# Kernel tuning notes

Hardware: AMD Instinct MI355X
Metric: run time of the kernel (lower is better)

## Reference

```python
import jax, jax.numpy as jnp
import numpy as np

B, S, D_MODEL, H = 256, 128, 1024, 8
DK = D_MODEL // H      # 128; source code implicitly requires S == DK == P
P = 128                # number of relative positions (2k+1)
SCALE = 1.0 / np.sqrt(DK * 3.0)  # scale_factor = 3 (c2c + p2c + c2p all present)
NEG = -1.0e9


def setup_inputs() -> dict:
    rng = jax.random.key(0)
    ks = jax.random.split(rng, 16)
    n = lambda k, sh, s=1.0: jax.random.normal(k, sh, dtype=jnp.float32) * s
    return {
        "query": n(ks[0], (B, S, D_MODEL)),
        "key": n(ks[1], (B, S, D_MODEL)),
        "value": n(ks[2], (B, S, D_MODEL)),
        "q_pos_indices": jax.random.randint(ks[3], (B, H, S, S), 0, P, dtype=jnp.int32),
        "kv_pos_indices": jax.random.randint(ks[4], (B, H, S, S), 0, P, dtype=jnp.int32),
        "rel_q": n(ks[5], (1, H, P, DK), 0.02),
        "rel_k": n(ks[6], (1, H, P, DK), 0.02),
        "rel_v": n(ks[7], (1, H, P, DK), 0.02),
        "Wq": n(ks[8], (D_MODEL, D_MODEL), 0.02), "bq": jnp.zeros((D_MODEL,), jnp.float32),
        "Wk": n(ks[9], (D_MODEL, D_MODEL), 0.02), "bk": jnp.zeros((D_MODEL,), jnp.float32),
        "Wv": n(ks[10], (D_MODEL, D_MODEL), 0.02), "bv": jnp.zeros((D_MODEL,), jnp.float32),
        "Wo": n(ks[11], (D_MODEL, D_MODEL), 0.02), "bo": jnp.zeros((D_MODEL,), jnp.float32),
    }


def _forward(query, key, value, q_pos, kv_pos, rel_q, rel_k, rel_v,
             Wq, bq, Wk, bk, Wv, bv, Wo, bo):
    def split(x):  # [B,S,D] -> [B,H,S,DK]
        return x.reshape(B, S, H, DK).transpose(0, 2, 1, 3)

    q = split(query @ Wq + bq)
    k = split(key @ Wk + bk)
    v = split(value @ Wv + bv)

    # content-to-content
    c2c = jnp.einsum('bhid,bhjd->bhij', q, k) * SCALE
    # position-to-content: rel_q @ k^T -> [B,H,P,S], gather over P with q_pos
    p2c = jnp.einsum('hpd,bhjd->bhpj', rel_q[0], k) * SCALE
    p2c = jnp.take_along_axis(p2c, q_pos, axis=2)          # [B,H,S,S]
    # content-to-position: q @ rel_k^T -> [B,H,S,P], gather over P with kv_pos
    c2p = jnp.einsum('bhid,hpd->bhip', q, rel_k[0]) * SCALE
    c2p = jnp.take_along_axis(c2p, kv_pos, axis=3)         # [B,H,S,S]

    scores = c2c + p2c + c2p
    # source subtracts (detached) rowwise max BEFORE masking
    scores = scores - jax.lax.stop_gradient(scores.max(axis=-1, keepdims=True))

    # mask = (pos_indices == 0), with first seq_len flattened entries (row 0) forced True;
    # masked_fill(mask == 0, -1e9) keeps entries where mask is True
    mask = (q_pos == 0)
    mask = mask.at[:, :, 0, :].set(True)
    scores = jnp.where(mask, scores, NEG)

    probs = jax.nn.softmax(scores, axis=-1)  # dropout inactive (eval / p=0)

    ctx = jnp.einsum('bhij,bhjd->bhid', probs, v)          # [B,H,S,DK]
    # value-side positional path (valid because P == S == DK in this module)
    pos_ctx = jnp.einsum('bhij,hjd->bhid', probs, rel_v[0])
    pos_ctx = jnp.take_along_axis(pos_ctx, kv_pos, axis=3)
    ctx = ctx + pos_ctx

    out = ctx.transpose(0, 2, 1, 3).reshape(B, S, D_MODEL)
    return out @ Wo + bo


def reference(query, key, value, q_pos_indices, kv_pos_indices, rel_q, rel_k, rel_v,
              Wq, bq, Wk, bk, Wv, bv, Wo, bo):
    return _forward(query, key, value, q_pos_indices, kv_pos_indices,
                    rel_q, rel_k, rel_v, Wq, bq, Wk, bk, Wv, bv, Wo, bo)
```

## Files before the change

### kernel.cpp

```cpp
#include <hip/hip_runtime.h>
#include <cstdint>
#include <cstddef>

typedef __bf16 bf16;
typedef __attribute__((ext_vector_type(8))) __bf16 bf16x8;
typedef __attribute__((ext_vector_type(4))) float f32x4;

#define NB 256
#define NS 128
#define NH 8
#define NDK 128
#define NP 128
#define NDM 1024

static constexpr float kScale = 0.05103103630798287f;
static constexpr float kNeg = -1.0e9f;

static __device__ __forceinline__ f32x4 mfma16(bf16x8 a, bf16x8 b, f32x4 c) {
  return __builtin_amdgcn_mfma_f32_16x16x32_bf16(a, b, c, 0, 0, 0);
}

static __device__ __forceinline__ void gld_lds16(const bf16* g, bf16* l) {
  __builtin_amdgcn_global_load_lds(
      (const __attribute__((address_space(1))) void*)g,
      (__attribute__((address_space(3))) void*)l, 16, 0, 0);
}

static __device__ __forceinline__ float red16_max(float v) {
  v = fmaxf(v, __shfl_xor(v, 1, 64));
  v = fmaxf(v, __shfl_xor(v, 2, 64));
  v = fmaxf(v, __shfl_xor(v, 4, 64));
  v = fmaxf(v, __shfl_xor(v, 8, 64));
  return v;
}
static __device__ __forceinline__ float red16_sum(float v) {
  v += __shfl_xor(v, 1, 64);
  v += __shfl_xor(v, 2, 64);
  v += __shfl_xor(v, 4, 64);
  v += __shfl_xor(v, 8, 64);
  return v;
}

static __device__ void transpose64(const float* __restrict__ src, bf16* __restrict__ dst,
                                   int rows, int cols, int r0, int c0,
                                   float (*t)[65], int tid) {
  const int tr = tid >> 4, tc = tid & 15;
#pragma unroll
  for (int i = 0; i < 4; i++) {
    int r = tr + i * 16;
    float4 v = *(const float4*)&src[(size_t)(r0 + r) * cols + c0 + tc * 4];
    t[r][tc * 4 + 0] = v.x;
    t[r][tc * 4 + 1] = v.y;
    t[r][tc * 4 + 2] = v.z;
    t[r][tc * 4 + 3] = v.w;
  }
  __syncthreads();
#pragma unroll
  for (int i = 0; i < 4; i++) {
    int c = tr + i * 16;
    union { bf16 o[4]; uint64_t u; } pk;
#pragma unroll
    for (int k2 = 0; k2 < 4; k2++) pk.o[k2] = (bf16)t[tc * 4 + k2][c];
    *(uint64_t*)&dst[(size_t)(c0 + c) * rows + r0 + tc * 4] = pk.u;
  }
}

__global__ __launch_bounds__(256) void prep_kernel(
    const float* __restrict__ Wq, const float* __restrict__ Wk,
    const float* __restrict__ Wv, const float* __restrict__ Wo,
    const float* __restrict__ rel_q, const float* __restrict__ rel_k,
    const float* __restrict__ rel_v,
    bf16* __restrict__ Wtq, bf16* __restrict__ Wtk,
    bf16* __restrict__ Wtv, bf16* __restrict__ Wto,
    bf16* __restrict__ rqb, bf16* __restrict__ rkb, bf16* __restrict__ rvt) {
  __shared__ float t[64][65];
  const int tid = threadIdx.x;
  const int z = blockIdx.z;
  if (z < 4) {
    const float* src = (z == 0) ? Wq : (z == 1) ? Wk : (z == 2) ? Wv : Wo;
    bf16* dst = (z == 0) ? Wtq : (z == 1) ? Wtk : (z == 2) ? Wtv : Wto;
    transpose64(src, dst, NDM, NDM, blockIdx.y * 64, blockIdx.x * 64, t, tid);
  } else if (z == 4) {
    int lb = blockIdx.y * 16 + blockIdx.x;
    if (lb < 32) {
      int hh = lb >> 2, tt = lb & 3;
      transpose64(rel_v + (size_t)hh * NP * NDK, rvt + (size_t)hh * NDK * NP,
                  NP, NDK, (tt >> 1) * 64, (tt & 1) * 64, t, tid);
    }
  } else {
    int lb = blockIdx.y * 16 + blockIdx.x;
    if (lb < 128) {
      size_t base = (size_t)lb * 1024 + (size_t)tid * 4;
      float4 a = *(const float4*)&rel_q[base];
      float4 c = *(const float4*)&rel_k[base];
      union { bf16 o[4]; uint64_t u; } pa, pc;
      pa.o[0] = (bf16)a.x; pa.o[1] = (bf16)a.y; pa.o[2] = (bf16)a.z; pa.o[3] = (bf16)a.w;
      pc.o[0] = (bf16)c.x; pc.o[1] = (bf16)c.y; pc.o[2] = (bf16)c.z; pc.o[3] = (bf16)c.w;
      *(uint64_t*)&rqb[base] = pa.u;
      *(uint64_t*)&rkb[base] = pc.u;
    }
  }
}

__global__ __launch_bounds__(256) void cast_kernel(
    const float* __restrict__ x0, const float* __restrict__ x1,
    const float* __restrict__ x2,
    bf16* __restrict__ y0, bf16* __restrict__ y1, bf16* __restrict__ y2) {
  const int z = blockIdx.z;
  const float* x = (z == 0) ? x0 : (z == 1) ? x1 : x2;
  bf16* y = (z == 0) ? y0 : (z == 1) ? y1 : y2;
  size_t i = ((size_t)blockIdx.x * 256 + threadIdx.x) * 8;
  float4 a = *(const float4*)&x[i];
  float4 b = *(const float4*)&x[i + 4];
  union { bf16 o[8]; bf16x8 v; } u;
  u.o[0] = (bf16)a.x; u.o[1] = (bf16)a.y; u.o[2] = (bf16)a.z; u.o[3] = (bf16)a.w;
  u.o[4] = (bf16)b.x; u.o[5] = (bf16)b.y; u.o[6] = (bf16)b.z; u.o[7] = (bf16)b.w;
  *(bf16x8*)&y[i] = u.v;
}

__global__ __launch_bounds__(256) void proj_gemm(
    const bf16* __restrict__ Xq, const bf16* __restrict__ Xk, const bf16* __restrict__ Xv,
    const bf16* __restrict__ Wtq, const bf16* __restrict__ Wtk, const bf16* __restrict__ Wtv,
    const float* __restrict__ bq, const float* __restrict__ bk, const float* __restrict__ bv,
    bf16* __restrict__ Oq, bf16* __restrict__ Ok, bf16* __restrict__ Ov) {
  __shared__ __attribute__((aligned(16))) bf16 sA[128 * 64];
  __shared__ __attribute__((aligned(16))) bf16 sB[128 * 64];
  const int z = blockIdx.z;
  const bf16* X = (z == 0) ? Xq : (z == 1) ? Xk : Xv;
  const bf16* Wt = (z == 0) ? Wtq : (z == 1) ? Wtk : Wtv;
  const float* bias = (z == 0) ? bq : (z == 1) ? bk : bv;
  bf16* O = (z == 0) ? Oq : (z == 1) ? Ok : Ov;

  const int M0 = blockIdx.y * 128, N0 = blockIdx.x * 128;
  const int tid = threadIdx.x, lane = tid & 63, w = tid >> 6;
  const int l15 = lane & 15, l4 = lane >> 4;
  const int wm = w >> 1, wn = w & 1;

  f32x4 acc[4][4];
#pragma unroll
  for (int mt = 0; mt < 4; mt++)
#pragma unroll
    for (int nt = 0; nt < 4; nt++) acc[mt][nt] = (f32x4){0.f, 0.f, 0.f, 0.f};

  const int lr = lane >> 3, lc = (lane & 7) * 8;
  const bf16* ap[4];
  const bf16* bp[4];
#pragma unroll
  for (int i = 0; i < 4; i++) {
    int row = w * 32 + i * 8 + lr;
    ap[i] = X + (size_t)(M0 + row) * NDM + lc;
    bp[i] = Wt + (size_t)(N0 + row) * NDM + lc;
  }

  for (int k0 = 0; k0 < NDM; k0 += 64) {
#pragma unroll
    for (int i = 0; i < 4; i++) {
      int chunk = w * 4 + i;
      gld_lds16(ap[i], sA + chunk * 512);
      gld_lds16(bp[i], sB + chunk * 512);
      ap[i] += 64;
      bp[i] += 64;
    }
    __syncthreads();
#pragma unroll
    for (int kk = 0; kk < 64; kk += 32) {
      bf16x8 af[4], bfv[4];
#pragma unroll
      for (int mt = 0; mt < 4; mt++)
        af[mt] = *(const bf16x8*)&sA[(wm * 64 + mt * 16 + l15) * 64 + kk + l4 * 8];
#pragma unroll
      for (int nt = 0; nt < 4; nt++)
        bfv[nt] = *(const bf16x8*)&sB[(wn * 64 + nt * 16 + l15) * 64 + kk + l4 * 8];
#pragma unroll
      for (int mt = 0; mt < 4; mt++)
#pragma unroll
        for (int nt = 0; nt < 4; nt++)
          acc[mt][nt] = mfma16(af[mt], bfv[nt], acc[mt][nt]);
    }
    __syncthreads();
  }
#pragma unroll
  for (int mt = 0; mt < 4; mt++) {
#pragma unroll
    for (int nt = 0; nt < 4; nt++) {
      int n = N0 + wn * 64 + nt * 16 + l15;
      float bv_ = bias[n];
      int h = n >> 7, dk = n & 127;
#pragma unroll
      for (int r = 0; r < 4; r++) {
        int m = M0 + wm * 64 + mt * 16 + l4 * 4 + r;
        int b = m >> 7, s = m & 127;
        O[(((size_t)b * NH + h) * NS + s) * NDK + dk] = (bf16)(acc[mt][nt][r] + bv_);
      }
    }
  }
}

__global__ __launch_bounds__(256) void out_gemm(
    const bf16* __restrict__ Ax, const bf16* __restrict__ Wt,
    const float* __restrict__ bias, float* __restrict__ Out) {
  __shared__ __attribute__((aligned(16))) bf16 sA[128 * 64];
  __shared__ __attribute__((aligned(16))) bf16 sB[128 * 64];
  const int M0 = blockIdx.y * 128, N0 = blockIdx.x * 128;
  const int tid = threadIdx.x, lane = tid & 63, w = tid >> 6;
  const int l15 = lane & 15, l4 = lane >> 4;
  const int wm = w >> 1, wn = w & 1;

  f32x4 acc[4][4];
#pragma unroll
  for (int mt = 0; mt < 4; mt++)
#pragma unroll
    for (int nt = 0; nt < 4; nt++) acc[mt][nt] = (f32x4){0.f, 0.f, 0.f, 0.f};

  const int lr = lane >> 3, lc = (lane & 7) * 8;
  const bf16* ap[4];
  const bf16* bp[4];
#pragma unroll
  for (int i = 0; i < 4; i++) {
    int row = w * 32 + i * 8 + lr;
    ap[i] = Ax + (size_t)(M0 + row) * NDM + lc;
    bp[i] = Wt + (size_t)(N0 + row) * NDM + lc;
  }

  for (int k0 = 0; k0 < NDM; k0 += 64) {
#pragma unroll
    for (int i = 0; i < 4; i++) {
      int chunk = w * 4 + i;
      gld_lds16(ap[i], sA + chunk * 512);
      gld_lds16(bp[i], sB + chunk * 512);
      ap[i] += 64;
      bp[i] += 64;
    }
    __syncthreads();
#pragma unroll
    for (int kk = 0; kk < 64; kk += 32) {
      bf16x8 af[4], bfv[4];
#pragma unroll
      for (int mt = 0; mt < 4; mt++)
        af[mt] = *(const bf16x8*)&sA[(wm * 64 + mt * 16 + l15) * 64 + kk + l4 * 8];
#pragma unroll
      for (int nt = 0; nt < 4; nt++)
        bfv[nt] = *(const bf16x8*)&sB[(wn * 64 + nt * 16 + l15) * 64 + kk + l4 * 8];
#pragma unroll
      for (int mt = 0; mt < 4; mt++)
#pragma unroll
        for (int nt = 0; nt < 4; nt++)
          acc[mt][nt] = mfma16(af[mt], bfv[nt], acc[mt][nt]);
    }
    __syncthreads();
  }
#pragma unroll
  for (int mt = 0; mt < 4; mt++) {
#pragma unroll
    for (int nt = 0; nt < 4; nt++) {
      int n = N0 + wn * 64 + nt * 16 + l15;
      float bv_ = bias[n];
#pragma unroll
      for (int r = 0; r < 4; r++) {
        int m = M0 + wm * 64 + mt * 16 + l4 * 4 + r;
        Out[(size_t)m * NDM + n] = acc[mt][nt][r] + bv_;
      }
    }
  }
}

__global__ __launch_bounds__(256) void vt_kernel(const bf16* __restrict__ Vin,
                                                 bf16* __restrict__ Vt) {
  __shared__ __attribute__((aligned(16))) bf16 t[64][72];
  const size_t base = (size_t)blockIdx.z * (NS * NDK);
  const int r0 = blockIdx.y * 64, c0 = blockIdx.x * 64;
  const int tid = threadIdx.x;
  const int tr = tid >> 3, tc8 = tid & 7;
#pragma unroll
  for (int i = 0; i < 2; i++) {
    int r = tr + i * 32;
    *(bf16x8*)&t[r][tc8 * 8] = *(const bf16x8*)&Vin[base + (size_t)(r0 + r) * NDK + c0 + tc8 * 8];
  }
  __syncthreads();
#pragma unroll
  for (int i = 0; i < 2; i++) {
    int c = tr + i * 32;
    bf16x8 o;
#pragma unroll
    for (int k2 = 0; k2 < 8; k2++) o[k2] = t[tc8 * 8 + k2][c];
    *(bf16x8*)&Vt[base + (size_t)(c0 + c) * NS + r0 + tc8 * 8] = o;
  }
}

__global__ __launch_bounds__(256, 1) void attn_kernel(
    const bf16* __restrict__ Qg, const bf16* __restrict__ Kg, const bf16* __restrict__ Vtg,
    const bf16* __restrict__ relq, const bf16* __restrict__ relk, const bf16* __restrict__ relvT,
    const int* __restrict__ qpos, const int* __restrict__ kvpos,
    bf16* __restrict__ ctx) {
  constexpr int LD = 136;
  __shared__ __attribute__((aligned(16))) bf16 R0[128 * LD];
  __shared__ __attribute__((aligned(16))) bf16 R1[128 * LD];
  __shared__ __attribute__((aligned(16))) bf16 R2[128 * LD];
  __shared__ __attribute__((aligned(16))) bf16 R3[128 * LD];

  const int bh = blockIdx.x;
  const int b = bh >> 3, h = bh & 7;
  const int tid = threadIdx.x, lane = tid & 63, w = tid >> 6;
  const int l15 = lane & 15, l4 = lane >> 4;
  const int m0 = w * 32;

  const size_t tb = (size_t)bh * (NS * NDK);
  const bf16* Qp = Qg + tb;
  const bf16* Kp = Kg + tb;
  const bf16* Vp = Vtg + tb;
  const bf16* rq = relq + (size_t)h * NP * NDK;
  const bf16* rk = relk + (size_t)h * NP * NDK;
  const bf16* rv = relvT + (size_t)h * NDK * NP;
  const int* qpp = qpos + (size_t)bh * NS * NS;
  const int* kpp = kvpos + (size_t)bh * NS * NS;

  auto load_tile = [&](bf16* dst, const bf16* src) {
    const int r = tid >> 4, c8 = tid & 15;
#pragma unroll
    for (int i = 0; i < 8; i++) {
      int rr = r + i * 16;
      *(bf16x8*)&dst[rr * LD + c8 * 8] = *(const bf16x8*)&src[rr * 128 + c8 * 8];
    }
  };
  auto gemmNT = [&](const bf16* A, const bf16* Bm, f32x4 (&acc)[2][8]) {
#pragma unroll
    for (int kk = 0; kk < 128; kk += 32) {
      bf16x8 a0 = *(const bf16x8*)&A[(m0 + l15) * LD + kk + l4 * 8];
      bf16x8 a1 = *(const bf16x8*)&A[(m0 + 16 + l15) * LD + kk + l4 * 8];
#pragma unroll
      for (int nt = 0; nt < 8; nt++) {
        bf16x8 bb = *(const bf16x8*)&Bm[(nt * 16 + l15) * LD + kk + l4 * 8];
        acc[0][nt] = mfma16(a0, bb, acc[0][nt]);
        acc[1][nt] = mfma16(a1, bb, acc[1][nt]);
      }
    }
  };

  load_tile(R0, Qp);
  load_tile(R1, Kp);
  load_tile(R2, rq);
  __syncthreads();

  {
    f32x4 acc[2][8];
#pragma unroll
    for (int mt = 0; mt < 2; mt++)
#pragma unroll
      for (int nt = 0; nt < 8; nt++) acc[mt][nt] = (f32x4){0.f, 0.f, 0.f, 0.f};
    gemmNT(R2, R1, acc);
#pragma unroll
    for (int mt = 0; mt < 2; mt++)
#pragma unroll
      for (int nt = 0; nt < 8; nt++)
#pragma unroll
        for (int r = 0; r < 4; r++) {
          int pp = m0 + mt * 16 + l4 * 4 + r;
          int j = nt * 16 + l15;
          R3[pp * LD + j] = (bf16)(acc[mt][nt][r] * kScale);
        }
  }
  f32x4 sc[2][8];
#pragma unroll
  for (int mt = 0; mt < 2; mt++)
#pragma unroll
    for (int nt = 0; nt < 8; nt++) sc[mt][nt] = (f32x4){0.f, 0.f, 0.f, 0.f};
  gemmNT(R0, R1, sc);
  __syncthreads();

  load_tile(R2, rk);
  __syncthreads();

  {
    f32x4 acc[2][8];
#pragma unroll
    for (int mt = 0; mt < 2; mt++)
#pragma unroll
      for (int nt = 0; nt < 8; nt++) acc[mt][nt] = (f32x4){0.f, 0.f, 0.f, 0.f};
    gemmNT(R0, R2, acc);
#pragma unroll
    for (int mt = 0; mt < 2; mt++)
#pragma unroll
      for (int nt = 0; nt < 8; nt++)
#pragma unroll
        for (int r = 0; r < 4; r++) {
          int i = m0 + mt * 16 + l4 * 4 + r;
          int pp = nt * 16 + l15;
          R1[i * LD + pp] = (bf16)(acc[mt][nt][r] * kScale);
        }
  }

  unsigned long long keep = 0ull;
#pragma unroll
  for (int mt = 0; mt < 2; mt++)
#pragma unroll
    for (int nt = 0; nt < 8; nt++)
#pragma unroll
      for (int r = 0; r < 4; r++) {
        int i = m0 + mt * 16 + l4 * 4 + r;
        int j = nt * 16 + l15;
        int qv = qpp[i * NS + j];
        int kv = kpp[i * NS + j];
        float v = sc[mt][nt][r] * kScale + (float)R3[qv * LD + j] + (float)R1[i * LD + kv];
        sc[mt][nt][r] = v;
        if (qv == 0 || i == 0) keep |= 1ull << (mt * 32 + nt * 4 + r);
      }
  float rmx[2][4];
#pragma unroll
  for (int mt = 0; mt < 2; mt++)
#pragma unroll
    for (int r = 0; r < 4; r++) {
      float m = -3.0e38f;
#pragma unroll
      for (int nt = 0; nt < 8; nt++) m = fmaxf(m, sc[mt][nt][r]);
      rmx[mt][r] = red16_max(m);
    }
#pragma unroll
  for (int mt = 0; mt < 2; mt++)
#pragma unroll
    for (int nt = 0; nt < 8; nt++)
#pragma unroll
      for (int r = 0; r < 4; r++) {
        float v = sc[mt][nt][r] - rmx[mt][r];
        if (!((keep >> (mt * 32 + nt * 4 + r)) & 1ull)) v = kNeg;
        sc[mt][nt][r] = v;
      }
  float m2[2][4], inv[2][4];
#pragma unroll
  for (int mt = 0; mt < 2; mt++)
#pragma unroll
    for (int r = 0; r < 4; r++) {
      float m = -3.0e38f;
#pragma unroll
      for (int nt = 0; nt < 8; nt++) m = fmaxf(m, sc[mt][nt][r]);
      m2[mt][r] = red16_max(m);
    }
#pragma unroll
  for (int mt = 0; mt < 2; mt++)
#pragma unroll
    for (int nt = 0; nt < 8; nt++)
#pragma unroll
      for (int r = 0; r < 4; r++) sc[mt][nt][r] = __expf(sc[mt][nt][r] - m2[mt][r]);
#pragma unroll
  for (int mt = 0; mt < 2; mt++)
#pragma unroll
    for (int r = 0; r < 4; r++) {
      float s = 0.f;
#pragma unroll
      for (int nt = 0; nt < 8; nt++) s += sc[mt][nt][r];
      inv[mt][r] = 1.0f / red16_sum(s);
    }
#pragma unroll
  for (int mt = 0; mt < 2; mt++)
#pragma unroll
    for (int nt = 0; nt < 8; nt++)
#pragma unroll
      for (int r = 0; r < 4; r++) sc[mt][nt][r] *= inv[mt][r];
  __syncthreads();

#pragma unroll
  for (int mt = 0; mt < 2; mt++)
#pragma unroll
    for (int nt = 0; nt < 8; nt++)
#pragma unroll
      for (int r = 0; r < 4; r++) {
        int i = m0 + mt * 16 + l4 * 4 + r;
        int j = nt * 16 + l15;
        R3[i * LD + j] = (bf16)sc[mt][nt][r];
      }
  load_tile(R0, Vp);
  load_tile(R1, rv);
  __syncthreads();

  {
    f32x4 acc2[2][8];
#pragma unroll
    for (int mt = 0; mt < 2; mt++)
#pragma unroll
      for (int nt = 0; nt < 8; nt++) acc2[mt][nt] = (f32x4){0.f, 0.f, 0.f, 0.f};
    gemmNT(R3, R1, acc2);
#pragma unroll
    for (int mt = 0; mt < 2; mt++)
#pragma unroll
      for (int nt = 0; nt < 8; nt++)
#pragma unroll
        for (int r = 0; r < 4; r++) {
          int i = m0 + mt * 16 + l4 * 4 + r;
          int d = nt * 16 + l15;
          R2[i * LD + d] = (bf16)acc2[mt][nt][r];
        }
  }
  {
    f32x4 acc1[2][8];
#pragma unroll
    for (int mt = 0; mt < 2; mt++)
#pragma unroll
      for (int nt = 0; nt < 8; nt++) acc1[mt][nt] = (f32x4){0.f, 0.f, 0.f, 0.f};
    gemmNT(R3, R0, acc1);
#pragma unroll
    for (int mt = 0; mt < 2; mt++)
#pragma unroll
      for (int nt = 0; nt < 8; nt++)
#pragma unroll
        for (int r = 0; r < 4; r++) {
          int i = m0 + mt * 16 + l4 * 4 + r;
          int d = nt * 16 + l15;
          int kv = kpp[i * NS + d];
          float v = acc1[mt][nt][r] + (float)R2[i * LD + kv];
          ctx[(((size_t)b * NS + i) * NH + h) * NDK + d] = (bf16)v;
        }
  }
}

extern "C" void kernel_launch(void* const* d_in, const int* in_sizes, int n_in,
                              void* d_out, int out_size, void* d_ws, size_t ws_size,
                              hipStream_t stream) {
  const float* query = (const float*)d_in[0];
  const float* key   = (const float*)d_in[1];
  const float* value = (const float*)d_in[2];
  const int* qpos    = (const int*)d_in[3];
  const int* kvpos   = (const int*)d_in[4];
  const float* rel_q = (const float*)d_in[5];
  const float* rel_k = (const float*)d_in[6];
  const float* rel_v = (const float*)d_in[7];
  const float* Wq = (const float*)d_in[8];
  const float* bq = (const float*)d_in[9];
  const float* Wk = (const float*)d_in[10];
  const float* bk = (const float*)d_in[11];
  const float* Wv = (const float*)d_in[12];
  const float* bv = (const float*)d_in[13];
  const float* Wo = (const float*)d_in[14];
  const float* bo = (const float*)d_in[15];
  float* out = (float*)d_out;

  char* p = (char*)d_ws;
  size_t off = 0;
  auto take = [&](size_t n) {
    char* r = p + off;
    off += (n + 255) & ~(size_t)255;
    return r;
  };
  bf16* Wtq = (bf16*)take((size_t)NDM * NDM * 2);
  bf16* Wtk = (bf16*)take((size_t)NDM * NDM * 2);
  bf16* Wtv = (bf16*)take((size_t)NDM * NDM * 2);
  bf16* Wto = (bf16*)take((size_t)NDM * NDM * 2);
  bf16* rqb = (bf16*)take((size_t)NH * NP * NDK * 2);
  bf16* rkb = (bf16*)take((size_t)NH * NP * NDK * 2);
  bf16* rvt = (bf16*)take((size_t)NH * NDK * NP * 2);
  const size_t big = (size_t)NB * NH * NS * NDK * 2;
  bf16* qws  = (bf16*)take(big);
  bf16* kws  = (bf16*)take(big);
  bf16* vws  = (bf16*)take(big);
  bf16* vtws = (bf16*)take(big);
  bf16* ctxw = (bf16*)take(big);
  bf16* xtra = (bf16*)take(big);
  bf16* xq = vtws;
  bf16* xk = ctxw;
  bf16* xv = xtra;

  hipLaunchKernelGGL(prep_kernel, dim3(16, 16, 6), dim3(256), 0, stream,
                     Wq, Wk, Wv, Wo, rel_q, rel_k, rel_v,
                     Wtq, Wtk, Wtv, Wto, rqb, rkb, rvt);
  hipLaunchKernelGGL(cast_kernel, dim3((NB * NS * NDM) / (256 * 8), 1, 3), dim3(256), 0, stream,
                     query, key, value, xq, xk, xv);
  hipLaunchKernelGGL(proj_gemm, dim3(8, 256, 3), dim3(256), 0, stream,
                     xq, xk, xv, Wtq, Wtk, Wtv, bq, bk, bv, qws, kws, vws);
  hipLaunchKernelGGL(vt_kernel, dim3(2, 2, NB * NH), dim3(256), 0, stream, vws, vtws);
  hipLaunchKernelGGL(attn_kernel, dim3(NB * NH), dim3(256), 0, stream,
                     qws, kws, vtws, rqb, rkb, rvt, qpos, kvpos, ctxw);
  hipLaunchKernelGGL(out_gemm, dim3(8, 256), dim3(256), 0, stream, ctxw, Wto, bo, out);
}
```

Measured before the change: 1.210 ms.

## Replace projection and output GEMMs with 256x256 double-buffered pipelined kernel

Merges the two GEMM kernels into one templated kernel that uses 256x256 tiles, 512 threads, and double-buffered LDS. Global loads for the next tile are interleaved between MFMA phases, with explicit waitcnt, barriers and setprio. It also XOR-swizzles the LDS layout to avoid bank conflicts and remaps block order so neighbouring blocks share L2 data. The aim is more operand reuse and overlap of memory with compute, at the cost of heavy register pressure and many barriers.

```diff
diff --git a/kernel.cpp b/kernel.cpp
--- a/kernel.cpp
+++ b/kernel.cpp
@@ -24,6 +24,12 @@
   __builtin_amdgcn_global_load_lds(
       (const __attribute__((address_space(1))) void*)g,
       (__attribute__((address_space(3))) void*)l, 16, 0, 0);
+}
+
+static __device__ __forceinline__ void barx() {
+  __builtin_amdgcn_sched_barrier(0);
+  __builtin_amdgcn_s_barrier();
+  __builtin_amdgcn_sched_barrier(0);
 }
 
 static __device__ __forceinline__ float red16_max(float v) {
@@ -118,147 +124,165 @@
   *(bf16x8*)&y[i] = u.v;
 }
 
-__global__ __launch_bounds__(256) void proj_gemm(
-    const bf16* __restrict__ Xq, const bf16* __restrict__ Xk, const bf16* __restrict__ Xv,
-    const bf16* __restrict__ Wtq, const bf16* __restrict__ Wtk, const bf16* __restrict__ Wtv,
-    const float* __restrict__ bq, const float* __restrict__ bk, const float* __restrict__ bv,
-    bf16* __restrict__ Oq, bf16* __restrict__ Ok, bf16* __restrict__ Ov) {
-  __shared__ __attribute__((aligned(16))) bf16 sA[128 * 64];
-  __shared__ __attribute__((aligned(16))) bf16 sB[128 * 64];
+#define TSZ (256 * 64)
+
+template <int MODE>
+__global__ __launch_bounds__(512, 2) void gemm256(
+    const bf16* __restrict__ X0, const bf16* __restrict__ X1, const bf16* __restrict__ X2,
+    const bf16* __restrict__ W0, const bf16* __restrict__ W1, const bf16* __restrict__ W2,
+    const float* __restrict__ b0p, const float* __restrict__ b1p, const float* __restrict__ b2p,
+    bf16* __restrict__ Obf0, bf16* __restrict__ Obf1, bf16* __restrict__ Obf2,
+    float* __restrict__ Of32) {
+  __shared__ __attribute__((aligned(16))) bf16 sA[2 * TSZ];
+  __shared__ __attribute__((aligned(16))) bf16 sB[2 * TSZ];
+
   const int z = blockIdx.z;
-  const bf16* X = (z == 0) ? Xq : (z == 1) ? Xk : Xv;
-  const bf16* Wt = (z == 0) ? Wtq : (z == 1) ? Wtk : Wtv;
-  const float* bias = (z == 0) ? bq : (z == 1) ? bk : bv;
-  bf16* O = (z == 0) ? Oq : (z == 1) ? Ok : Ov;
-
-  const int M0 = blockIdx.y * 128, N0 = blockIdx.x * 128;
+  const bf16* X  = (MODE == 1) ? X0 : ((z == 0) ? X0 : (z == 1) ? X1 : X2);
+  const bf16* Wt = (MODE == 1) ? W0 : ((z == 0) ? W0 : (z == 1) ? W1 : W2);
+  const float* bias = (MODE == 1) ? b0p : ((z == 0) ? b0p : (z == 1) ? b1p : b2p);
+
+  const int nx = gridDim.x;
+  const int flat = blockIdx.y * nx + blockIdx.x;
+  const int cpx = (nx * gridDim.y) >> 3;
+  const int swz = (flat & 7) * cpx + (flat >> 3);
+  const int M0 = (swz / nx) * 256;
+  const int N0 = (swz % nx) * 256;
+
   const int tid = threadIdx.x, lane = tid & 63, w = tid >> 6;
   const int l15 = lane & 15, l4 = lane >> 4;
-  const int wm = w >> 1, wn = w & 1;
-
-  f32x4 acc[4][4];
-#pragma unroll
-  for (int mt = 0; mt < 4; mt++)
+  const int wm = w >> 2, wn = w & 3;
+
+  const int lr = lane >> 3;
+  const int scol = ((lane & 7) ^ lr) * 8;
+  const size_t aRow = (size_t)(M0 + w * 16 + lr) * NDM + scol;
+  const size_t bRow = (size_t)(N0 + w * 16 + lr) * NDM + scol;
+  bf16* const dA = sA + (w * 16) * 64;
+  bf16* const dB = sB + (w * 16) * 64;
+
+  auto stA = [&](int bufi, int half, int t) {
+    const bf16* s = X + aRow + (size_t)half * 128 * NDM + t * 64;
+    bf16* d = dA + bufi * TSZ + half * (128 * 64);
+    gld_lds16(s, d);
+    gld_lds16(s + 8 * NDM, d + 8 * 64);
+  };
+  auto stB = [&](int bufi, int half, int t) {
+    const bf16* s = Wt + bRow + (size_t)half * 128 * NDM + t * 64;
+    bf16* d = dB + bufi * TSZ + half * (128 * 64);
+    gld_lds16(s, d);
+    gld_lds16(s + 8 * NDM, d + 8 * 64);
+  };
+
+  f32x4 acc[8][4];
+#pragma unroll
+  for (int mt = 0; mt < 8; mt++)
 #pragma unroll
     for (int nt = 0; nt < 4; nt++) acc[mt][nt] = (f32x4){0.f, 0.f, 0.f, 0.f};
 
-  const int lr = lane >> 3, lc = (lane & 7) * 8;
-  const bf16* ap[4];
-  const bf16* bp[4];
-#pragma unroll
-  for (int i = 0; i < 4; i++) {
-    int row = w * 32 + i * 8 + lr;
-    ap[i] = X + (size_t)(M0 + row) * NDM + lc;
-    bp[i] = Wt + (size_t)(N0 + row) * NDM + lc;
-  }
-
-  for (int k0 = 0; k0 < NDM; k0 += 64) {
-#pragma unroll
-    for (int i = 0; i < 4; i++) {
-      int chunk = w * 4 + i;
-      gld_lds16(ap[i], sA + chunk * 512);
-      gld_lds16(bp[i], sB + chunk * 512);
-      ap[i] += 64;
-      bp[i] += 64;
-    }
-    __syncthreads();
-#pragma unroll
-    for (int kk = 0; kk < 64; kk += 32) {
-      bf16x8 af[4], bfv[4];
-#pragma unroll
-      for (int mt = 0; mt < 4; mt++)
-        af[mt] = *(const bf16x8*)&sA[(wm * 64 + mt * 16 + l15) * 64 + kk + l4 * 8];
-#pragma unroll
-      for (int nt = 0; nt < 4; nt++)
-        bfv[nt] = *(const bf16x8*)&sB[(wn * 64 + nt * 16 + l15) * 64 + kk + l4 * 8];
-#pragma unroll
-      for (int mt = 0; mt < 4; mt++)
-#pragma unroll
-        for (int nt = 0; nt < 4; nt++)
-          acc[mt][nt] = mfma16(af[mt], bfv[nt], acc[mt][nt]);
-    }
-    __syncthreads();
-  }
-#pragma unroll
-  for (int mt = 0; mt < 4; mt++) {
-#pragma unroll
-    for (int nt = 0; nt < 4; nt++) {
-      int n = N0 + wn * 64 + nt * 16 + l15;
-      float bv_ = bias[n];
-      int h = n >> 7, dk = n & 127;
-#pragma unroll
-      for (int r = 0; r < 4; r++) {
-        int m = M0 + wm * 64 + mt * 16 + l4 * 4 + r;
-        int b = m >> 7, s = m & 127;
-        O[(((size_t)b * NH + h) * NS + s) * NDK + dk] = (bf16)(acc[mt][nt][r] + bv_);
+  const int kc0 = (l4 * 8) ^ ((l15 & 7) * 8);
+  const int kc1 = (32 + l4 * 8) ^ ((l15 & 7) * 8);
+  int arow[8], brow[4];
+#pragma unroll
+  for (int mt = 0; mt < 8; mt++) arow[mt] = (wm * 128 + mt * 16 + l15) * 64;
+#pragma unroll
+  for (int nt = 0; nt < 4; nt++) brow[nt] = (wn * 64 + nt * 16 + l15) * 64;
+
+  stA(0, 0, 0); stA(0, 1, 0); stB(0, 0, 0); stB(0, 1, 0);
+
+  const int NT = NDM / 64;
+  for (int t = 0; t < NT; ++t) {
+    const int cur = t & 1, nxt = cur ^ 1;
+    const bf16* cA = sA + cur * TSZ;
+    const bf16* cB = sB + cur * TSZ;
+    const bool pf = (t + 1 < NT);
+
+    if (pf) {
+      stA(nxt, 0, t + 1);
+      asm volatile("s_waitcnt vmcnt(2)" ::: "memory");
+    } else {
+      asm volatile("s_waitcnt vmcnt(0)" ::: "memory");
+    }
+    barx();
+    bf16x8 a0[8], b0[4], a1[8], b1[4];
+#pragma unroll
+    for (int mt = 0; mt < 4; mt++) a0[mt] = *(const bf16x8*)&cA[arow[mt] + kc0];
+#pragma unroll
+    for (int nt = 0; nt < 4; nt++) b0[nt] = *(const bf16x8*)&cB[brow[nt] + kc0];
+#pragma unroll
+    for (int mt = 4; mt < 8; mt++) a0[mt] = *(const bf16x8*)&cA[arow[mt] + kc0];
+    __builtin_amdgcn_s_setprio(1);
+#pragma unroll
+    for (int mt = 0; mt < 4; mt++)
+#pragma unroll
+      for (int nt = 0; nt < 4; nt++) acc[mt][nt] = mfma16(a0[mt], b0[nt], acc[mt][nt]);
+    __builtin_amdgcn_s_setprio(0);
+    barx();
+
+#pragma unroll
+    for (int mt = 0; mt < 4; mt++) a1[mt] = *(const bf16x8*)&cA[arow[mt] + kc1];
+    if (pf) stA(nxt, 1, t + 1);
+    barx();
+    __builtin_amdgcn_s_setprio(1);
+#pragma unroll
+    for (int mt = 4; mt < 8; mt++)
+#pragma unroll
+      for (int nt = 0; nt < 4; nt++) acc[mt][nt] = mfma16(a0[mt], b0[nt], acc[mt][nt]);
+    __builtin_amdgcn_s_setprio(0);
+    barx();
+
+#pragma unroll
+    for (int nt = 0; nt < 4; nt++) b1[nt] = *(const bf16x8*)&cB[brow[nt] + kc1];
+#pragma unroll
+    for (int mt = 4; mt < 8; mt++) a1[mt] = *(const bf16x8*)&cA[arow[mt] + kc1];
+    if (pf) stB(nxt, 0, t + 1);
+    barx();
+    __builtin_amdgcn_s_setprio(1);
+#pragma unroll
+    for (int mt = 0; mt < 4; mt++)
+#pragma unroll
+      for (int nt = 0; nt < 4; nt++) acc[mt][nt] = mfma16(a1[mt], b1[nt], acc[mt][nt]);
+    __builtin_amdgcn_s_setprio(0);
+    barx();
+
+    if (pf) stB(nxt, 1, t + 1);
+    barx();
+    __builtin_amdgcn_s_setprio(1);
+#pragma unroll
+    for (int mt = 4; mt < 8; mt++)
+#pragma unroll
+      for (int nt = 0; nt < 4; nt++) acc[mt][nt] = mfma16(a1[mt], b1[nt], acc[mt][nt]);
+    __builtin_amdgcn_s_setprio(0);
+    barx();
+  }
+
+  if (MODE == 0) {
+    bf16* O = (z == 0) ? Obf0 : (z == 1) ? Obf1 : Obf2;
+#pragma unroll
+    for (int mt = 0; mt < 8; mt++) {
+#pragma unroll
+      for (int nt = 0; nt < 4; nt++) {
+        const int n = N0 + wn * 64 + nt * 16 + l15;
+        const float bv_ = bias[n];
+        const int h = n >> 7, dk = n & 127;
+#pragma unroll
+        for (int r = 0; r < 4; r++) {
+          const int m = M0 + wm * 128 + mt * 16 + l4 * 4 + r;
+          const int b = m >> 7, s = m & 127;
+          O[(((size_t)b * NH + h) * NS + s) * NDK + dk] = (bf16)(acc[mt][nt][r] + bv_);
+        }
       }
     }
-  }
-}
-
-__global__ __launch_bounds__(256) void out_gemm(
-    const bf16* __restrict__ Ax, const bf16* __restrict__ Wt,
-    const float* __restrict__ bias, float* __restrict__ Out) {
-  __shared__ __attribute__((aligned(16))) bf16 sA[128 * 64];
-  __shared__ __attribute__((aligned(16))) bf16 sB[128 * 64];
-  const int M0 = blockIdx.y * 128, N0 = blockIdx.x * 128;
-  const int tid = threadIdx.x, lane = tid & 63, w = tid >> 6;
-  const int l15 = lane & 15, l4 = lane >> 4;
-  const int wm = w >> 1, wn = w & 1;
-
-  f32x4 acc[4][4];
-#pragma unroll
-  for (int mt = 0; mt < 4; mt++)
-#pragma unroll
-    for (int nt = 0; nt < 4; nt++) acc[mt][nt] = (f32x4){0.f, 0.f, 0.f, 0.f};
-
-  const int lr = lane >> 3, lc = (lane & 7) * 8;
-  const bf16* ap[4];
-  const bf16* bp[4];
-#pragma unroll
-  for (int i = 0; i < 4; i++) {
-    int row = w * 32 + i * 8 + lr;
-    ap[i] = Ax + (size_t)(M0 + row) * NDM + lc;
-    bp[i] = Wt + (size_t)(N0 + row) * NDM + lc;
-  }
-
-  for (int k0 = 0; k0 < NDM; k0 += 64) {
-#pragma unroll
-    for (int i = 0; i < 4; i++) {
-      int chunk = w * 4 + i;
-      gld_lds16(ap[i], sA + chunk * 512);
-      gld_lds16(bp[i], sB + chunk * 512);
-      ap[i] += 64;
-      bp[i] += 64;
-    }
-    __syncthreads();
-#pragma unroll
-    for (int kk = 0; kk < 64; kk += 32) {
-      bf16x8 af[4], bfv[4];
-#pragma unroll
-      for (int mt = 0; mt < 4; mt++)
-        af[mt] = *(const bf16x8*)&sA[(wm * 64 + mt * 16 + l15) * 64 + kk + l4 * 8];
-#pragma unroll
-      for (int nt = 0; nt < 4; nt++)
-        bfv[nt] = *(const bf16x8*)&sB[(wn * 64 + nt * 16 + l15) * 64 + kk + l4 * 8];
-#pragma unroll
-      for (int mt = 0; mt < 4; mt++)
-#pragma unroll
-        for (int nt = 0; nt < 4; nt++)
-          acc[mt][nt] = mfma16(af[mt], bfv[nt], acc[mt][nt]);
-    }
-    __syncthreads();
-  }
-#pragma unroll
-  for (int mt = 0; mt < 4; mt++) {
-#pragma unroll
-    for (int nt = 0; nt < 4; nt++) {
-      int n = N0 + wn * 64 + nt * 16 + l15;
-      float bv_ = bias[n];
-#pragma unroll
-      for (int r = 0; r < 4; r++) {
-        int m = M0 + wm * 64 + mt * 16 + l4 * 4 + r;
-        Out[(size_t)m * NDM + n] = acc[mt][nt][r] + bv_;
+  } else {
+#pragma unroll
+    for (int mt = 0; mt < 8; mt++) {
+#pragma unroll
+      for (int nt = 0; nt < 4; nt++) {
+        const int n = N0 + wn * 64 + nt * 16 + l15;
+        const float bv_ = bias[n];
+#pragma unroll
+        for (int r = 0; r < 4; r++) {
+          const int m = M0 + wm * 128 + mt * 16 + l4 * 4 + r;
+          Of32[(size_t)m * NDM + n] = acc[mt][nt][r] + bv_;
+        }
       }
     }
   }
@@ -562,10 +586,14 @@
                      Wtq, Wtk, Wtv, Wto, rqb, rkb, rvt);
   hipLaunchKernelGGL(cast_kernel, dim3((NB * NS * NDM) / (256 * 8), 1, 3), dim3(256), 0, stream,
                      query, key, value, xq, xk, xv);
-  hipLaunchKernelGGL(proj_gemm, dim3(8, 256, 3), dim3(256), 0, stream,
-                     xq, xk, xv, Wtq, Wtk, Wtv, bq, bk, bv, qws, kws, vws);
+  hipLaunchKernelGGL((gemm256<0>), dim3(4, 128, 3), dim3(512), 0, stream,
+                     xq, xk, xv, Wtq, Wtk, Wtv, bq, bk, bv, qws, kws, vws, (float*)nullptr);
   hipLaunchKernelGGL(vt_kernel, dim3(2, 2, NB * NH), dim3(256), 0, stream, vws, vtws);
   hipLaunchKernelGGL(attn_kernel, dim3(NB * NH), dim3(256), 0, stream,
                      qws, kws, vtws, rqb, rkb, rvt, qpos, kvpos, ctxw);
-  hipLaunchKernelGGL(out_gemm, dim3(8, 256), dim3(256), 0, stream, ctxw, Wto, bo, out);
-}
+  hipLaunchKernelGGL((gemm256<1>), dim3(4, 128, 1), dim3(512), 0, stream,
+                     ctxw, (const bf16*)nullptr, (const bf16*)nullptr,
+                     Wto, (const bf16*)nullptr, (const bf16*)nullptr,
+                     bo, (const float*)nullptr, (const float*)nullptr,
+                     (bf16*)nullptr, (bf16*)nullptr, (bf16*)nullptr, out);
+}
```

New measurement: 1.129 ms. 6.6% less time.
